# Optimization experiments

Measured on AMD Instinct MI355X. Metric: run time of the kernel, lower is better.

## Reference

```python
import jax, jax.numpy as jnp
import numpy as np

DEGREE = 5
A = 1.0
B = 1.0
IN_F = 1024
OUT_F = 1024
BATCH = 8192


def setup_inputs() -> dict:
    key = jax.random.key(0)
    k1, k2, k3, k4 = jax.random.split(key, 4)
    x = jax.random.normal(k1, (BATCH, IN_F), dtype=jnp.float32)
    # base_weight ~ kaiming-uniform-ish scale
    bound_w = 1.0 / np.sqrt(IN_F)
    base_weight = jax.random.uniform(k2, (OUT_F, IN_F), dtype=jnp.float32,
                                     minval=-bound_w, maxval=bound_w)
    std = 1.0 / (IN_F * np.sqrt(DEGREE + 1))
    jacobi_coeffs = std * jax.random.normal(k3, (OUT_F, IN_F, DEGREE + 1), dtype=jnp.float32)
    bias = jax.random.uniform(k4, (OUT_F,), dtype=jnp.float32, minval=-bound_w, maxval=bound_w)
    return {"x": x, "base_weight": base_weight, "jacobi_coeffs": jacobi_coeffs, "bias": bias}


def _jacobi_polynomials(x):
    # x: (batch, in_features) -> (batch, in_features, DEGREE+1)
    t = jnp.tanh(x)
    polys = [jnp.ones_like(t)]
    if DEGREE >= 1:
        polys.append(0.5 * (2.0 * (A + 1.0) * t + (A - B)))
    for k in range(2, DEGREE + 1):
        # recurrence coefficients (matching torch loop where k = written index)
        alpha_n = 2.0 * k * (k + A + B) * (2 * k + A + B - 2)
        beta_n = (2 * k + A + B - 1) * (A ** 2 - B ** 2)
        gamma_n = (2 * k + A + B - 2) * (2 * k + A + B - 1) * (2 * k + A + B)
        delta_n = 2.0 * (k + A - 1) * (k + B - 1) * (2 * k + A + B)
        Acoef = (beta_n + alpha_n * t) / gamma_n
        Bcoef = delta_n / gamma_n
        polys.append(Acoef * polys[k - 1] - Bcoef * polys[k - 2])
    return jnp.stack(polys, axis=-1)


def reference(x, base_weight, jacobi_coeffs, bias):
    # base branch: SiLU then linear
    base_out = jax.nn.silu(x) @ base_weight.T  # (b, out)
    # jacobi branch
    P = _jacobi_polynomials(x)  # (b, in, deg+1)
    jac_out = jnp.einsum('bik,oik->bo', P, jacobi_coeffs)
    return base_out + jac_out + bias
```

## Files before the change

### kernel.cpp

```cpp
#include <hip/hip_runtime.h>
#include <hip/hip_bf16.h>
#include <cstdint>
#include <cstddef>

#define BATCH   8192
#define IN_F    1024
#define OUT_F   1024
#define KAUG    (6 * 1024)
#define NSTEP   64

typedef __bf16 bf16x8 __attribute__((ext_vector_type(8)));
typedef float  f32x4  __attribute__((ext_vector_type(4)));

static constexpr size_t WAUG_B    = (size_t)OUT_F * KAUG * 2;
static constexpr size_t BIAS2_OFF = WAUG_B;

constexpr float M1_1 = 2.0f;
constexpr float M3_1 = -1.0714285714f;
constexpr float M5_1 =  0.5812890813f;
constexpr float M2_2 =  1.0666666667f;
constexpr float M4_2 = -1.0455026455f;
constexpr float M3_3 =  0.5714285714f;
constexpr float M5_3 = -0.8141735129f;
constexpr float M4_4 =  0.3047619048f;
constexpr float M5_5 =  0.1616161616f;
constexpr float M2_0 = -0.4f;
constexpr float M4_0 =  0.1777777778f;

__device__ __forceinline__ unsigned short f2bf(float f)
{
    __hip_bfloat16 h = __float2bfloat16(f);
    return *(unsigned short*)&h;
}
__device__ __forceinline__ unsigned pack2(float lo, float hi)
{
    return (unsigned)f2bf(lo) | ((unsigned)f2bf(hi) << 16);
}
__device__ __forceinline__ unsigned cvt_pk(float lo, float hi)
{
    unsigned r;
    asm("v_cvt_pk_bf16_f32 %0, %1, %2" : "=v"(r) : "v"(lo), "v"(hi));
    return r;
}

__global__ void prep_w(const float* __restrict__ W,
                       const float* __restrict__ C,
                       const float* __restrict__ bias,
                       __hip_bfloat16* __restrict__ Waug,
                       float* __restrict__ bias2)
{
    const int o = blockIdx.x;
    const int tid = threadIdx.x;

    __shared__ __align__(16) float cs[IN_F * 6];
    __shared__ float red[4];

    const float4* C4  = (const float4*)(C + (size_t)o * IN_F * 6);
    float4*       cs4 = (float4*)cs;
#pragma unroll
    for (int k = 0; k < 6; ++k) cs4[tid + k * 256] = C4[tid + k * 256];

    const float4 wv = ((const float4*)(W + (size_t)o * IN_F))[tid];
    const float w4[4] = {wv.x, wv.y, wv.z, wv.w};

    __syncthreads();

    float f[24];
#pragma unroll
    for (int q = 0; q < 6; ++q) {
        const float4 v = cs4[tid * 6 + q];
        f[q * 4 + 0] = v.x; f[q * 4 + 1] = v.y; f[q * 4 + 2] = v.z; f[q * 4 + 3] = v.w;
    }

    unsigned pk[12];
    float s = 0.f;
#pragma unroll
    for (int q = 0; q < 4; ++q) {
        const float c0 = f[q * 6 + 0], c1 = f[q * 6 + 1], c2 = f[q * 6 + 2];
        const float c3 = f[q * 6 + 3], c4 = f[q * 6 + 4], c5 = f[q * 6 + 5];
        const float cp1 = M1_1 * c1 + M3_1 * c3 + M5_1 * c5;
        const float cp2 = M2_2 * c2 + M4_2 * c4;
        const float cp3 = M3_3 * c3 + M5_3 * c5;
        const float cp4 = M4_4 * c4;
        const float cp5 = M5_5 * c5;
        s += c0 + M2_0 * c2 + M4_0 * c4;
        pk[q * 3 + 0] = pack2(w4[q], cp1);
        pk[q * 3 + 1] = pack2(cp2,   cp3);
        pk[q * 3 + 2] = pack2(cp4,   cp5);
    }

#pragma unroll
    for (int off = 32; off > 0; off >>= 1) s += __shfl_down(s, off, 64);
    if ((tid & 63) == 0) red[tid >> 6] = s;

    __syncthreads();
    uint4* csU = (uint4*)cs;
    csU[tid * 3 + 0] = make_uint4(pk[0], pk[1], pk[2],  pk[3]);
    csU[tid * 3 + 1] = make_uint4(pk[4], pk[5], pk[6],  pk[7]);
    csU[tid * 3 + 2] = make_uint4(pk[8], pk[9], pk[10], pk[11]);
    __syncthreads();

    uint4* out4 = (uint4*)(Waug + (size_t)o * KAUG);
#pragma unroll
    for (int k = 0; k < 3; ++k) out4[tid + k * 256] = csU[tid + k * 256];

    if (tid == 0) bias2[o] = bias[o] + red[0] + red[1] + red[2] + red[3];
}

__device__ __forceinline__ void async_load16(const void* g, void* l)
{
    __builtin_amdgcn_global_load_lds(
        (const __attribute__((address_space(1))) void*)g,
        (__attribute__((address_space(3))) void*)l,
        16, 0, 0);
}

#define AS_B    26624
#define BS_B    24576
#define SMEM_B  (AS_B + 2 * BS_B)

__global__ __launch_bounds__(256, 2)
void gemm_kan(const float* __restrict__ X,
              const __hip_bfloat16* __restrict__ Waug,
              const float* __restrict__ bias2,
              float* __restrict__ out)
{
    extern __shared__ __align__(16) char smem[];

    const int tid  = threadIdx.x;
    const int lane = tid & 63;
    const int wave = tid >> 6;
    const int wm = wave & 1, wn = wave >> 1;
    const int mBase = blockIdx.x * 128;
    const int nBase = blockIdx.y * 128;

    const float* gx = X + (size_t)(mBase + (tid >> 1)) * IN_F + (tid & 1) * 8;
    char* const aw = smem + (tid >> 1) * 208 + (tid & 1) * 96;

    const __hip_bfloat16* gB[6]; int lB[6];
#pragma unroll
    for (int q = 0; q < 6; ++q) {
        const int ci = (q * 4 + wave) * 64 + lane;
        const int br = ci / 12, bc = ci - br * 12;
        gB[q] = Waug + (size_t)(nBase + br) * KAUG + bc * 8;
        lB[q] = AS_B + (q * 4 + wave) * 1024;
    }

    const int quad = lane >> 4, mr = lane & 15;
    const int aoff = (wm * 64 + mr) * 13 + quad;
    const int boff = (AS_B / 16) + (wn * 64 + mr) * 12 + quad;

    f32x4 acc[4][4] = {};

    float4 xc0 = *(const float4*)(gx);
    float4 xc1 = *(const float4*)(gx + 4);
#pragma unroll
    for (int q = 0; q < 6; ++q) async_load16(gB[q], smem + lB[q]);

#pragma unroll 1
    for (int t = 0; t < NSTEP; ++t) {
        const float xs[8] = {xc0.x, xc0.y, xc0.z, xc0.w, xc1.x, xc1.y, xc1.z, xc1.w};
        unsigned pk[24];
#pragma unroll
        for (int e = 0; e < 8; ++e) {
            const float x  = xs[e];
            const float v  = __expf(fminf(-x, 43.f));
            const float sg = __builtin_amdgcn_rcpf(1.f + v);
            const float s  = x * sg;
            const float u  = v * v;
            const float tt = (1.f - u) * __builtin_amdgcn_rcpf(1.f + u);
            const float t2 = tt * tt;
            const float t3 = t2 * tt;
            const float t4 = t2 * t2;
            const float t5 = t4 * tt;
            pk[e * 3 + 0] = cvt_pk(s,  tt);
            pk[e * 3 + 1] = cvt_pk(t2, t3);
            pk[e * 3 + 2] = cvt_pk(t4, t5);
        }
        __syncthreads();
#pragma unroll
        for (int j = 0; j < 6; ++j)
            *(uint4*)(aw + j * 16) = make_uint4(pk[j * 4], pk[j * 4 + 1],
                                                pk[j * 4 + 2], pk[j * 4 + 3]);
        __syncthreads();

        if (t + 1 < NSTEP) {
            char* const bs = smem + ((t + 1) & 1) * BS_B;
#pragma unroll
            for (int q = 0; q < 6; ++q) async_load16(gB[q] + (t + 1) * 96, bs + lB[q]);
            xc0 = *(const float4*)(gx + (t + 1) * 16);
            xc1 = *(const float4*)(gx + (t + 1) * 16 + 4);
        }

        const bf16x8* V = (const bf16x8*)smem;
        const int bo = boff + (t & 1) * (BS_B / 16);
#pragma unroll
        for (int kc = 0; kc < 3; ++kc) {
            bf16x8 a[4], b[4];
#pragma unroll
            for (int t4 = 0; t4 < 4; ++t4) a[t4] = V[aoff + t4 * 208 + kc * 4];
#pragma unroll
            for (int t4 = 0; t4 < 4; ++t4) b[t4] = V[bo + t4 * 192 + kc * 4];
#pragma unroll
            for (int i = 0; i < 4; ++i)
#pragma unroll
                for (int jj = 0; jj < 4; ++jj)
                    acc[i][jj] = __builtin_amdgcn_mfma_f32_16x16x32_bf16(a[i], b[jj], acc[i][jj], 0, 0, 0);
        }
    }

#pragma unroll
    for (int i = 0; i < 4; ++i) {
#pragma unroll
        for (int jj = 0; jj < 4; ++jj) {
            const int col = nBase + wn * 64 + jj * 16 + mr;
            const float b2 = bias2[col];
#pragma unroll
            for (int r = 0; r < 4; ++r) {
                const int row = mBase + wm * 64 + i * 16 + quad * 4 + r;
                out[(size_t)row * OUT_F + col] = acc[i][jj][r] + b2;
            }
        }
    }
}


extern "C" void kernel_launch(void* const* d_in, const int* in_sizes, int n_in,
                              void* d_out, int out_size, void* d_ws, size_t ws_size,
                              hipStream_t stream)
{
    (void)out_size; (void)ws_size;
    const float* x    = (const float*)d_in[0];
    const float* W    = (const float*)d_in[1];
    const float* C    = (const float*)d_in[2];
    const float* bias = (const float*)d_in[3];
    for (int i = 0; i < n_in; ++i) {
        if      (in_sizes[i] == BATCH * IN_F)     x    = (const float*)d_in[i];
        else if (in_sizes[i] == OUT_F * IN_F)     W    = (const float*)d_in[i];
        else if (in_sizes[i] == OUT_F * IN_F * 6) C    = (const float*)d_in[i];
        else if (in_sizes[i] == OUT_F)            bias = (const float*)d_in[i];
    }
    float* out = (float*)d_out;
    char* ws = (char*)d_ws;
    __hip_bfloat16* Waug  = (__hip_bfloat16*)ws;
    float*          bias2 = (float*)(ws + BIAS2_OFF);

    static bool smem_attr_done = false;
    if (!smem_attr_done) {
        (void)hipFuncSetAttribute((const void*)gemm_kan,
                                  hipFuncAttributeMaxDynamicSharedMemorySize,
                                  SMEM_B);
        smem_attr_done = true;
    }

    prep_w<<<dim3(OUT_F), dim3(256), 0, stream>>>(W, C, bias, Waug, bias2);
    gemm_kan<<<dim3(BATCH / 128, OUT_F / 128), dim3(256), SMEM_B, stream>>>(
        x, Waug, bias2, out);
}
```

Measured before the change: 223.8 us.

## Double-buffer the A tile, overlap basis compute with MFMA, enlarge the M tile

The GEMM block grows to 256x128 with 512 threads (8 waves), and the transformed-activation tile A is now double-buffered in LDS. SiLU/tanh-power computation for the next K-step runs after the current step's MFMAs, so only one barrier per iteration is needed instead of two. Each thread now issues half as many B async loads, and each B tile serves twice as many rows. LDS use rises to about 152KB per block, so only one block fits per CU. Wave count per CU stays the same, but there is less latency hiding across blocks.

New measurement: 210.0 us. 6.2% less time.

```diff
diff --git a/kernel.cpp b/kernel.cpp
--- a/kernel.cpp
+++ b/kernel.cpp
@@ -115,11 +115,12 @@
         16, 0, 0);
 }
 
-#define AS_B    26624
-#define BS_B    24576
-#define SMEM_B  (AS_B + 2 * BS_B)
-
-__global__ __launch_bounds__(256, 2)
+#define ASB_B   53248
+#define BSB_B   24576
+#define AS_TOT  (2 * ASB_B)
+#define SMEM_B  (AS_TOT + 2 * BSB_B)
+
+__global__ __launch_bounds__(512, 2)
 void gemm_kan(const float* __restrict__ X,
               const __hip_bfloat16* __restrict__ Waug,
               const float* __restrict__ bias2,
@@ -130,36 +131,34 @@
     const int tid  = threadIdx.x;
     const int lane = tid & 63;
     const int wave = tid >> 6;
-    const int wm = wave & 1, wn = wave >> 1;
-    const int mBase = blockIdx.x * 128;
+    const int wm = wave >> 1, wn = wave & 1;
+    const int mBase = blockIdx.x * 256;
     const int nBase = blockIdx.y * 128;
 
     const float* gx = X + (size_t)(mBase + (tid >> 1)) * IN_F + (tid & 1) * 8;
     char* const aw = smem + (tid >> 1) * 208 + (tid & 1) * 96;
 
-    const __hip_bfloat16* gB[6]; int lB[6];
-#pragma unroll
-    for (int q = 0; q < 6; ++q) {
-        const int ci = (q * 4 + wave) * 64 + lane;
+    const __hip_bfloat16* gB[3]; int lB[3];
+#pragma unroll
+    for (int q = 0; q < 3; ++q) {
+        const int ci = (q * 8 + wave) * 64 + lane;
         const int br = ci / 12, bc = ci - br * 12;
         gB[q] = Waug + (size_t)(nBase + br) * KAUG + bc * 8;
-        lB[q] = AS_B + (q * 4 + wave) * 1024;
+        lB[q] = AS_TOT + (q * 8 + wave) * 1024;
     }
 
     const int quad = lane >> 4, mr = lane & 15;
     const int aoff = (wm * 64 + mr) * 13 + quad;
-    const int boff = (AS_B / 16) + (wn * 64 + mr) * 12 + quad;
+    const int boff = (AS_TOT / 16) + (wn * 64 + mr) * 12 + quad;
 
     f32x4 acc[4][4] = {};
 
-    float4 xc0 = *(const float4*)(gx);
-    float4 xc1 = *(const float4*)(gx + 4);
-#pragma unroll
-    for (int q = 0; q < 6; ++q) async_load16(gB[q], smem + lB[q]);
-
-#pragma unroll 1
-    for (int t = 0; t < NSTEP; ++t) {
-        const float xs[8] = {xc0.x, xc0.y, xc0.z, xc0.w, xc1.x, xc1.y, xc1.z, xc1.w};
+    {
+#pragma unroll
+        for (int q = 0; q < 3; ++q) async_load16(gB[q], smem + lB[q]);
+        const float4 x0 = *(const float4*)(gx);
+        const float4 x1 = *(const float4*)(gx + 4);
+        const float xs[8] = {x0.x, x0.y, x0.z, x0.w, x1.x, x1.y, x1.z, x1.w};
         unsigned pk[24];
 #pragma unroll
         for (int e = 0; e < 8; ++e) {
@@ -169,44 +168,74 @@
             const float s  = x * sg;
             const float u  = v * v;
             const float tt = (1.f - u) * __builtin_amdgcn_rcpf(1.f + u);
-            const float t2 = tt * tt;
-            const float t3 = t2 * tt;
-            const float t4 = t2 * t2;
-            const float t5 = t4 * tt;
+            const float t2 = tt * tt, t3 = t2 * tt, t4 = t2 * t2, t5 = t4 * tt;
             pk[e * 3 + 0] = cvt_pk(s,  tt);
             pk[e * 3 + 1] = cvt_pk(t2, t3);
             pk[e * 3 + 2] = cvt_pk(t4, t5);
         }
-        __syncthreads();
 #pragma unroll
         for (int j = 0; j < 6; ++j)
             *(uint4*)(aw + j * 16) = make_uint4(pk[j * 4], pk[j * 4 + 1],
                                                 pk[j * 4 + 2], pk[j * 4 + 3]);
-        __syncthreads();
-
+    }
+    __syncthreads();
+
+#pragma unroll 1
+    for (int t = 0; t < NSTEP; ++t) {
         if (t + 1 < NSTEP) {
-            char* const bs = smem + ((t + 1) & 1) * BS_B;
-#pragma unroll
-            for (int q = 0; q < 6; ++q) async_load16(gB[q] + (t + 1) * 96, bs + lB[q]);
-            xc0 = *(const float4*)(gx + (t + 1) * 16);
-            xc1 = *(const float4*)(gx + (t + 1) * 16 + 4);
+            const int nsel = (t + 1) & 1;
+#pragma unroll
+            for (int q = 0; q < 3; ++q)
+                async_load16(gB[q] + (size_t)(t + 1) * 96,
+                             smem + lB[q] + nsel * BSB_B);
+        }
+        float4 xn0 = {}, xn1 = {};
+        if (t + 1 < NSTEP) {
+            xn0 = *(const float4*)(gx + (size_t)(t + 1) * 16);
+            xn1 = *(const float4*)(gx + (size_t)(t + 1) * 16 + 4);
         }
 
         const bf16x8* V = (const bf16x8*)smem;
-        const int bo = boff + (t & 1) * (BS_B / 16);
+        const int ab = aoff + (t & 1) * (ASB_B / 16);
+        const int bb = boff + (t & 1) * (BSB_B / 16);
 #pragma unroll
         for (int kc = 0; kc < 3; ++kc) {
             bf16x8 a[4], b[4];
 #pragma unroll
-            for (int t4 = 0; t4 < 4; ++t4) a[t4] = V[aoff + t4 * 208 + kc * 4];
-#pragma unroll
-            for (int t4 = 0; t4 < 4; ++t4) b[t4] = V[bo + t4 * 192 + kc * 4];
+            for (int t4 = 0; t4 < 4; ++t4) a[t4] = V[ab + t4 * 208 + kc * 4];
+#pragma unroll
+            for (int t4 = 0; t4 < 4; ++t4) b[t4] = V[bb + t4 * 192 + kc * 4];
 #pragma unroll
             for (int i = 0; i < 4; ++i)
 #pragma unroll
                 for (int jj = 0; jj < 4; ++jj)
-                    acc[i][jj] = __builtin_amdgcn_mfma_f32_16x16x32_bf16(a[i], b[jj], acc[i][jj], 0, 0, 0);
-        }
+                    acc[i][jj] = __builtin_amdgcn_mfma_f32_16x16x32_bf16(
+                        a[i], b[jj], acc[i][jj], 0, 0, 0);
+        }
+
+        if (t + 1 < NSTEP) {
+            const float xs[8] = {xn0.x, xn0.y, xn0.z, xn0.w, xn1.x, xn1.y, xn1.z, xn1.w};
+            unsigned pk[24];
+#pragma unroll
+            for (int e = 0; e < 8; ++e) {
+                const float x  = xs[e];
+                const float v  = __expf(fminf(-x, 43.f));
+                const float sg = __builtin_amdgcn_rcpf(1.f + v);
+                const float s  = x * sg;
+                const float u  = v * v;
+                const float tt = (1.f - u) * __builtin_amdgcn_rcpf(1.f + u);
+                const float t2 = tt * tt, t3 = t2 * tt, t4 = t2 * t2, t5 = t4 * tt;
+                pk[e * 3 + 0] = cvt_pk(s,  tt);
+                pk[e * 3 + 1] = cvt_pk(t2, t3);
+                pk[e * 3 + 2] = cvt_pk(t4, t5);
+            }
+            char* const asd = aw + ((t + 1) & 1) * ASB_B;
+#pragma unroll
+            for (int j = 0; j < 6; ++j)
+                *(uint4*)(asd + j * 16) = make_uint4(pk[j * 4], pk[j * 4 + 1],
+                                                     pk[j * 4 + 2], pk[j * 4 + 3]);
+        }
+        __syncthreads();
     }
 
 #pragma unroll
@@ -254,6 +283,6 @@
     }
 
     prep_w<<<dim3(OUT_F), dim3(256), 0, stream>>>(W, C, bias, Waug, bias2);
-    gemm_kan<<<dim3(BATCH / 128, OUT_F / 128), dim3(256), SMEM_B, stream>>>(
+    gemm_kan<<<dim3(BATCH / 256, OUT_F / 128), dim3(512), SMEM_B, stream>>>(
         x, Waug, bias2, out);
 }
```
